# Performance work log

Measured on AMD Instinct MI355X. Metric: run time of the kernel, lower is better.

The kernel has to match this reference:

```python
import jax, jax.numpy as jnp
import numpy as np

N, C, D, H, E, M = 4, 512, 768, 12, 20, 4   # docs, seq, hidden, heads, entities/doc, max mentions
EMB, BLK, L = 768, 64, 97                    # emb_size, block_size, num_labels
P = E * (E - 1)                              # ordered entity pairs per doc
NEG = -1e30


def _forward(seq, attn, mention_start, hts, Wm1, Wm2, bm, Watt, batt, Wpath, bpath,
             Whead, bhead, Wtail, btail, Wbil, bbil):
    def per_doc(seq_i, att_i, pos0, ht):
        pos = pos0 + 1                                            # BERT cls offset
        e_emb = seq_i[pos]                                        # [E,M,D] mention embeddings
        mean_att = att_i.mean(0)                                  # [C,C] head-mean attention
        e_att = jnp.pad(mean_att[pos], ((0, 0), (0, 0), (0, 1)))  # [E,M,C+1] zero pad col
        glob = jax.nn.logsumexp(e_emb, axis=1)                    # [E,D] entity glob emb
        hidx, tidx = ht[:, 0], ht[:, 1]
        hs = e_emb[hidx]; ts = e_emb[tidx]                        # [P,M,D]
        h_att = e_att[hidx]; t_att = e_att[tidx]                  # [P,M,C+1]
        ph = pos[hidx]; pt = pos[tidx]                            # [P,M]
        idx_t = jnp.broadcast_to(pt[:, None, :], (P, M, M))
        idx_h = jnp.broadcast_to(ph[:, None, :], (P, M, M))
        pair_hatt = jnp.take_along_axis(h_att, idx_t, axis=2).mean(1)  # [P,M]
        pair_tatt = jnp.take_along_axis(t_att, idx_h, axis=2).mean(1)
        pair_hatt = pair_hatt / (pair_hatt.sum(1, keepdims=True) + 1e-5)
        pair_tatt = pair_tatt / (pair_tatt.sum(1, keepdims=True) + 1e-5)
        new_hs = jnp.einsum('pm,pmd->pd', pair_tatt, hs)
        new_ts = jnp.einsum('pm,pmd->pd', pair_hatt, ts)
        nh_att = jnp.einsum('pm,pmc->pc', pair_tatt, h_att)
        nt_att = jnp.einsum('pm,pmc->pc', pair_hatt, t_att)
        pa = nh_att * nt_att
        pa = pa / (pa.sum(1, keepdims=True) + 1e-5)
        rs = pa[:, :C] @ seq_i                                    # [P,D] local context
        # RelEdgeLayer over fully-connected entity graph (eval-mode dropout = identity)
        A = glob @ Wm1; B = glob @ Wm2
        edge = jax.nn.relu(A[:, None, :] + B[None, :, :] + bm)    # [E,E,D] edge features
        # path attention: query = cat(hs,ts), targets = cat(e[h,v],e[v,t],e[t,v],e[v,h])
        q = jnp.concatenate([new_hs, new_ts], -1)                 # [P,2D]
        qW = q @ Watt                                             # [P,4D] bilinear half
        q1, q2, q3, q4 = jnp.split(qW, 4, axis=-1)
        E1 = edge[hidx]                                           # edge[h,v]  [P,E,D]
        E2 = jnp.swapaxes(edge[:, tidx], 0, 1)                    # edge[v,t]
        E3 = edge[tidx]                                           # edge[t,v]
        E4 = jnp.swapaxes(edge[:, hidx], 0, 1)                    # edge[v,h]
        score = (jnp.einsum('pd,pvd->pv', q1, E1) + jnp.einsum('pd,pvd->pv', q2, E2)
                 + jnp.einsum('pd,pvd->pv', q3, E3) + jnp.einsum('pd,pvd->pv', q4, E4) + batt)
        v_ids = jnp.arange(E)
        mask = (v_ids[None, :] == hidx[:, None]) | (v_ids[None, :] == tidx[:, None])
        aw = jax.nn.softmax(jnp.where(mask, NEG, score), axis=-1)  # [P,E]
        path = jnp.concatenate([jnp.einsum('pv,pvd->pd', aw, Ek) for Ek in (E1, E2, E3, E4)], -1)
        return new_hs, new_ts, rs, path

    nh, nt, rs, path = jax.vmap(per_doc)(seq, attn, mention_start, hts)
    nh = nh.reshape(-1, D); nt = nt.reshape(-1, D)
    rs = rs.reshape(-1, D); path = path.reshape(-1, 4 * D)
    path = jax.nn.relu(path @ Wpath + bpath)
    hs = jax.nn.relu(jnp.concatenate([nh, rs, path], -1) @ Whead + bhead)
    ts = jax.nn.relu(jnp.concatenate([nt, rs, path], -1) @ Wtail + btail)
    b1 = hs.reshape(-1, EMB // BLK, BLK)
    b2 = ts.reshape(-1, EMB // BLK, BLK)
    bl = (b1[:, :, :, None] * b2[:, :, None, :]).reshape(-1, EMB * BLK)
    return bl @ Wbil + bbil                                       # [N*P, L] logits


def setup_inputs() -> dict:
    key = jax.random.key(0)
    ks = jax.random.split(key, 16)
    s = 0.02
    pairs = np.array([(i, j) for i in range(E) for j in range(E) if i != j], dtype=np.int32)
    return {
        'sequence_output': jax.random.normal(ks[0], (N, C, D), jnp.float32),
        'attention': jax.random.uniform(ks[1], (N, H, C, C), jnp.float32),
        'mention_start': jax.random.randint(ks[2], (N, E, M), 0, C - 2),
        'hts': jnp.broadcast_to(jnp.asarray(pairs), (N, P, 2)),
        'Wm1': jax.random.normal(ks[3], (D, D)) * s,
        'Wm2': jax.random.normal(ks[4], (D, D)) * s,
        'bm': jnp.zeros((D,), jnp.float32),
        'Watt': jax.random.normal(ks[5], (2 * D, 4 * D)) * s,
        'batt': jnp.zeros((), jnp.float32),
        'Wpath': jax.random.normal(ks[6], (4 * D, D)) * s,
        'bpath': jnp.zeros((D,), jnp.float32),
        'Whead': jax.random.normal(ks[7], (3 * D, EMB)) * s,
        'bhead': jnp.zeros((EMB,), jnp.float32),
        'Wtail': jax.random.normal(ks[8], (3 * D, EMB)) * s,
        'btail': jnp.zeros((EMB,), jnp.float32),
        'Wbil': jax.random.normal(ks[9], (EMB * BLK, L)) * s,
        'bbil': jnp.zeros((L,), jnp.float32),
    }


def reference(sequence_output, attention, mention_start, hts, Wm1, Wm2, bm, Watt, batt,
              Wpath, bpath, Whead, bhead, Wtail, btail, Wbil, bbil):
    return _forward(sequence_output, attention, mention_start, hts, Wm1, Wm2, bm, Watt,
                    batt, Wpath, bpath, Whead, bhead, Wtail, btail, Wbil, bbil)
```

## Files before the change

### kernel.cpp

```cpp
#include <hip/hip_runtime.h>
#include <hip/hip_bf16.h>

#define NDOC 4
#define CL   512
#define DD   768
#define HH   12
#define EE   20
#define MM   4
#define PP   380
#define NPAIR 1520
#define LOUT 97
#define KP   40
#define KP2  72

typedef unsigned short u16;
typedef short bf16x8 __attribute__((ext_vector_type(8)));
typedef u16   u16x8  __attribute__((ext_vector_type(8)));
typedef u16   u16x4  __attribute__((ext_vector_type(4)));
typedef float f32x4  __attribute__((ext_vector_type(4)));

#define Z8 (u16x8){0,0,0,0,0,0,0,0}

__device__ __forceinline__ u16 f2bf(float x){
    union { float f; unsigned u; } v; v.f = x;
    return (u16)((v.u + 0x7fffu + ((v.u >> 16) & 1u)) >> 16);
}
__device__ __forceinline__ float bf2f(u16 h){
    union { unsigned u; float f; } v; v.u = ((unsigned)h) << 16;
    return v.f;
}
__device__ __forceinline__ void splitf(float x, u16 &h, u16 &l){
    h = f2bf(x);
    l = f2bf(x - bf2f(h));
}

__global__ __launch_bounds__(256) void k_wsplit(const float* __restrict__ W,
                                                u16* __restrict__ WH, u16* __restrict__ WL,
                                                int K, int N, long long srcStride,
                                                long long dstStride)
{
    __shared__ u16 tH[64][66], tL[64][66];
    const float* Wp = W + (size_t)blockIdx.z*srcStride;
    u16* WHp = WH + (size_t)blockIdx.z*dstStride;
    u16* WLp = WL + (size_t)blockIdx.z*dstStride;
    int n0 = blockIdx.x*64, k0 = blockIdx.y*64;
    int t = threadIdx.x;
    int kr = t>>4, c4 = (t&15)*4;
    bool vec4 = ((N & 3) == 0);
    #pragma unroll
    for (int rr=0; rr<4; ++rr) {
        int k = k0 + kr + rr*16;
        float arr[4];
        if (vec4 && n0 + c4 + 3 < N) {
            float4 v = *(const float4*)(Wp + (size_t)k*N + n0 + c4);
            arr[0]=v.x; arr[1]=v.y; arr[2]=v.z; arr[3]=v.w;
        } else {
            #pragma unroll
            for (int i=0;i<4;++i){ int n=n0+c4+i; arr[i] = (n<N)? Wp[(size_t)k*N+n] : 0.f; }
        }
        #pragma unroll
        for (int i=0;i<4;++i){
            u16 hh,ll; splitf(arr[i],hh,ll);
            tH[c4+i][kr+rr*16] = hh;
            tL[c4+i][kr+rr*16] = ll;
        }
    }
    __syncthreads();
    int nr = t>>4, kc = (t&15)*4;
    #pragma unroll
    for (int rr=0; rr<4; ++rr) {
        int nl = nr + rr*16;
        u16x4 vh, vl;
        #pragma unroll
        for (int i=0;i<4;++i){ vh[i]=tH[nl][kc+i]; vl[i]=tL[nl][kc+i]; }
        size_t o = (size_t)(n0+nl)*K + k0 + kc;
        *(u16x4*)(WHp + o) = vh;
        *(u16x4*)(WLp + o) = vl;
    }
}

__global__ __launch_bounds__(256) void k_prep(const float* __restrict__ att,
                                              const float* __restrict__ seq,
                                              const int* __restrict__ ms,
                                              float* __restrict__ eatt,
                                              float* __restrict__ glob)
{
    int b = blockIdx.x;
    if (b < NDOC*EE*MM) {
        int row = b;
        int i = row / (EE*MM);
        int pos = ms[row] + 1;
        const float* base = att + ((size_t)i*HH)*CL*CL + (size_t)pos*CL;
        for (int c = threadIdx.x; c < CL; c += 256) {
            float s = 0.f;
            #pragma unroll
            for (int h = 0; h < HH; ++h) s += base[(size_t)h*CL*CL + c];
            eatt[(size_t)row*CL + c] = s * (1.0f/HH);
        }
    } else {
        int ie = b - NDOC*EE*MM;
        int i = ie / EE;
        const int* mp = ms + ie*MM;
        const float* sb = seq + (size_t)i*CL*DD;
        const float* r0 = sb + (size_t)(mp[0]+1)*DD;
        const float* r1 = sb + (size_t)(mp[1]+1)*DD;
        const float* r2 = sb + (size_t)(mp[2]+1)*DD;
        const float* r3 = sb + (size_t)(mp[3]+1)*DD;
        for (int d = threadIdx.x; d < DD; d += 256) {
            float a=r0[d], bb=r1[d], c=r2[d], e=r3[d];
            float mx = fmaxf(fmaxf(a,bb), fmaxf(c,e));
            float s = expf(a-mx)+expf(bb-mx)+expf(c-mx)+expf(e-mx);
            glob[(size_t)ie*DD + d] = mx + logf(s);
        }
    }
}

__global__ __launch_bounds__(256) void k_pairvec(const float* __restrict__ seq,
                                                 const float* __restrict__ eatt,
                                                 const int* __restrict__ ms,
                                                 const int* __restrict__ hts,
                                                 u16* __restrict__ nhH, u16* __restrict__ nhL,
                                                 u16* __restrict__ ntH, u16* __restrict__ ntL,
                                                 u16* __restrict__ paH, u16* __restrict__ paL)
{
    int g = blockIdx.x;
    int i = g / PP;
    int h = hts[2*g], t = hts[2*g+1];
    const float* eh = eatt + (size_t)(i*EE+h)*MM*CL;
    const float* et = eatt + (size_t)(i*EE+t)*MM*CL;
    int ph[MM], pt[MM];
    #pragma unroll
    for (int m=0;m<MM;++m){ ph[m]=ms[(i*EE+h)*MM+m]+1; pt[m]=ms[(i*EE+t)*MM+m]+1; }
    float pH[MM], pT[MM]; float sh=0.f, st=0.f;
    #pragma unroll
    for (int m2=0; m2<MM; ++m2) {
        float s = 0.f, s2 = 0.f;
        #pragma unroll
        for (int m=0;m<MM;++m) { s += eh[m*CL + pt[m2]]; s2 += et[m*CL + ph[m2]]; }
        pH[m2] = s*0.25f;  sh += pH[m2];
        pT[m2] = s2*0.25f; st += pT[m2];
    }
    float rh = 1.f/(sh+1e-5f), rt = 1.f/(st+1e-5f);
    #pragma unroll
    for (int m=0;m<MM;++m){ pH[m]*=rh; pT[m]*=rt; }

    const float* sb = seq + (size_t)i*CL*DD;
    for (int d = threadIdx.x; d < DD; d += 256) {
        float nh = pT[0]*sb[(size_t)ph[0]*DD+d] + pT[1]*sb[(size_t)ph[1]*DD+d]
                 + pT[2]*sb[(size_t)ph[2]*DD+d] + pT[3]*sb[(size_t)ph[3]*DD+d];
        float nt = pH[0]*sb[(size_t)pt[0]*DD+d] + pH[1]*sb[(size_t)pt[1]*DD+d]
                 + pH[2]*sb[(size_t)pt[2]*DD+d] + pH[3]*sb[(size_t)pt[3]*DD+d];
        u16 hh,ll;
        splitf(nh,hh,ll);
        nhH[(size_t)g*DD + d]=hh; nhL[(size_t)g*DD + d]=ll;
        splitf(nt,hh,ll);
        ntH[(size_t)g*DD + d]=hh; ntL[(size_t)g*DD + d]=ll;
    }
    float vv[2]; float lsum = 0.f;
    #pragma unroll
    for (int it=0; it<2; ++it) {
        int c = threadIdx.x + it*256;
        float na = pT[0]*eh[c] + pT[1]*eh[CL+c] + pT[2]*eh[2*CL+c] + pT[3]*eh[3*CL+c];
        float nb = pH[0]*et[c] + pH[1]*et[CL+c] + pH[2]*et[2*CL+c] + pH[3]*et[3*CL+c];
        vv[it] = na*nb; lsum += vv[it];
    }
    float tot = lsum;
    #pragma unroll
    for (int o=32;o;o>>=1) tot += __shfl_xor(tot, o);
    __shared__ float wsum[4];
    if ((threadIdx.x & 63)==0) wsum[threadIdx.x>>6] = tot;
    __syncthreads();
    float inv = 1.f/(wsum[0]+wsum[1]+wsum[2]+wsum[3] + 1e-5f);
    #pragma unroll
    for (int it=0; it<2; ++it){
        int c = threadIdx.x + it*256;
        u16 hh,ll; splitf(vv[it]*inv,hh,ll);
        paH[(size_t)g*CL + c]=hh; paL[(size_t)g*CL + c]=ll;
    }
}

__global__ __launch_bounds__(256) void k_edge(const float* __restrict__ Ab,
                                              const float* __restrict__ Bb,
                                              const float* __restrict__ bm,
                                              float* __restrict__ edge)
{
    int iht = blockIdx.x;
    int i = iht/(EE*EE); int rem = iht%(EE*EE); int h = rem/EE; int tt = rem%EE;
    const float* a = Ab + (size_t)(i*EE+h)*DD;
    const float* b = Bb + (size_t)(i*EE+tt)*DD;
    float* e = edge + (size_t)iht*DD;
    for (int d=threadIdx.x; d<DD; d+=256)
        e[d] = fmaxf(a[d]+b[d]+bm[d], 0.f);
}

__global__ __launch_bounds__(256) void k_scorepath(const float* __restrict__ qW,
                                                   const float* __restrict__ edge,
                                                   const int* __restrict__ hts,
                                                   const float* __restrict__ battp,
                                                   u16* __restrict__ pathcH,
                                                   u16* __restrict__ pathcL)
{
    int g = blockIdx.x;
    int i = g / PP;
    int h = hts[2*g], t = hts[2*g+1];
    __shared__ float qs[4*DD];
    __shared__ float sc[EE];
    __shared__ float aw[EE];
    for (int d4 = threadIdx.x; d4 < DD; d4 += 256)
        *(float4*)&qs[d4*4] = *(const float4*)(qW + (size_t)g*3072 + d4*4);
    __syncthreads();
    const float* eb = edge + (size_t)i*EE*EE*DD;
    int lane = threadIdx.x & 63, wid = threadIdx.x >> 6;
    for (int v = wid; v < EE; v += 4) {
        const float* e1 = eb + (size_t)(h*EE+v)*DD;
        const float* e2 = eb + (size_t)(v*EE+t)*DD;
        const float* e3 = eb + (size_t)(t*EE+v)*DD;
        const float* e4 = eb + (size_t)(v*EE+h)*DD;
        float s = 0.f;
        for (int d = lane; d < DD; d += 64)
            s += qs[d]*e1[d] + qs[DD+d]*e2[d] + qs[2*DD+d]*e3[d] + qs[3*DD+d]*e4[d];
        #pragma unroll
        for (int o=32;o;o>>=1) s += __shfl_xor(s, o);
        if (lane==0) sc[v] = s + battp[0];
    }
    __syncthreads();
    if (threadIdx.x == 0) {
        float mx = -3.0e38f;
        for (int v=0;v<EE;++v){ float x = (v==h||v==t)? -1e30f : sc[v]; sc[v]=x; mx = fmaxf(mx,x); }
        float su=0.f;
        for (int v=0;v<EE;++v){ float e = expf(sc[v]-mx); aw[v]=e; su+=e; }
        float inv = 1.f/su;
        for (int v=0;v<EE;++v) aw[v]*=inv;
    }
    __syncthreads();
    for (int idx = threadIdx.x; idx < 4*DD; idx += 256) {
        int k = idx / DD, d = idx % DD;
        const float* e;
        int stride;
        if (k==0)      { e = eb + (size_t)h*EE*DD + d; stride = DD; }
        else if (k==1) { e = eb + (size_t)t*DD + d;     stride = EE*DD; }
        else if (k==2) { e = eb + (size_t)t*EE*DD + d;  stride = DD; }
        else           { e = eb + (size_t)h*DD + d;     stride = EE*DD; }
        float s = 0.f;
        #pragma unroll
        for (int v=0; v<EE; ++v) s += aw[v]*e[(size_t)v*stride];
        u16 hh,ll; splitf(s,hh,ll);
        pathcH[(size_t)g*3072 + idx] = hh;
        pathcL[(size_t)g*3072 + idx] = ll;
    }
}

__global__ __launch_bounds__(256) void gemm_f32s(const float* __restrict__ glob,
                                                 const float* __restrict__ W1,
                                                 const float* __restrict__ W2,
                                                 float* __restrict__ C1,
                                                 float* __restrict__ C2)
{
    int doc = blockIdx.z >> 1, sel = blockIdx.z & 1;
    const float* A = glob + (size_t)doc*EE*DD;
    const float* B = sel ? W2 : W1;
    float* C = (sel ? C2 : C1) + (size_t)doc*EE*DD;
    __shared__ float As[16][68];
    __shared__ float Bs[16][68];
    int n0 = blockIdx.x*64;
    int t = threadIdx.x;
    int tx = t & 15, ty = t >> 4;
    int am = t >> 2, ac = (t & 3) * 4;
    int bk = t >> 4, bn = (t & 15) * 4;
    float acc[4][4] = {};
    for (int k0 = 0; k0 < DD; k0 += 16) {
        float4 av = make_float4(0,0,0,0);
        if (am < EE) av = *reinterpret_cast<const float4*>(A + (size_t)am*DD + k0 + ac);
        As[ac+0][am]=av.x; As[ac+1][am]=av.y; As[ac+2][am]=av.z; As[ac+3][am]=av.w;
        float4 bv = *reinterpret_cast<const float4*>(B + (size_t)(k0+bk)*DD + n0 + bn);
        *reinterpret_cast<float4*>(&Bs[bk][bn]) = bv;
        __syncthreads();
        #pragma unroll
        for (int kk=0; kk<16; ++kk) {
            const float4 a = *reinterpret_cast<const float4*>(&As[kk][ty*4]);
            const float4 b = *reinterpret_cast<const float4*>(&Bs[kk][tx*4]);
            float ar[4] = {a.x,a.y,a.z,a.w};
            float br[4] = {b.x,b.y,b.z,b.w};
            #pragma unroll
            for (int r=0;r<4;++r)
                #pragma unroll
                for (int c2=0;c2<4;++c2) acc[r][c2] = fmaf(ar[r], br[c2], acc[r][c2]);
        }
        __syncthreads();
    }
    #pragma unroll
    for (int r=0;r<4;++r) {
        int gm = ty*4 + r;
        if (gm >= EE) continue;
        #pragma unroll
        for (int c2=0;c2<4;++c2)
            C[(size_t)gm*DD + n0 + tx*4 + c2] = acc[r][c2];
    }
}

enum { MQW=0, MSPLIT=1, MRS=2, MHT=3 };

template<int MODE, int BM, int BN>
__global__ __launch_bounds__(256) void gemm_mfma(
    const u16* __restrict__ aH0, const u16* __restrict__ aL0,
    const u16* __restrict__ aH1, const u16* __restrict__ aL1,
    const u16* __restrict__ aH2, const u16* __restrict__ aL2,
    const u16* __restrict__ a0bH, const u16* __restrict__ a0bL,
    const u16* __restrict__ bH, const u16* __restrict__ bL,
    const u16* __restrict__ bHb, const u16* __restrict__ bLb,
    const float* __restrict__ bias, const float* __restrict__ biasb,
    float* __restrict__ oF,
    u16* __restrict__ oH, u16* __restrict__ oL,
    u16* __restrict__ oHb, u16* __restrict__ oLb,
    int M, int N, int Ktot, int segsz)
{
    constexpr int NWN = BN/64;
    constexpr int NWM = 4/NWN;
    constexpr int WM  = BM/NWM;
    constexpr int MFR = WM/16;
    constexpr int NFR = 4;
    __shared__ u16 AsH[BM*KP], AsL[BM*KP], BsH[BN*KP], BsL[BN*KP];

    const int t = threadIdx.x;
    const int z = blockIdx.z;
    const int m0 = blockIdx.y*BM, n0 = blockIdx.x*BN;
    const int lane = t & 63, wid = t >> 6;
    const int wr = wid / NWN, wc = wid % NWN;
    const int lrow = lane & 15, lg = lane >> 4;

    const u16 *segH0=aH0, *segL0=aL0;
    const u16 *bHp = bH, *bLp = bL;
    const float* bp = bias;
    float* fOut = nullptr;
    u16 *hOut = oH, *lOut = oL;
    int Mloc = M;
    long long outRow0 = 0;
    if constexpr (MODE==MRS) {
        segH0 = aH0 + (size_t)z*PP*CL;  segL0 = aL0 + (size_t)z*PP*CL;
        bHp   = bH  + (size_t)z*DD*CL;  bLp   = bL  + (size_t)z*DD*CL;
        Mloc = PP; outRow0 = (long long)z*PP;
    }
    if constexpr (MODE==MHT) {
        if (z == 0) { fOut = oF; hOut = nullptr; lOut = nullptr; }
        else { segH0 = a0bH; segL0 = a0bL; bHp = bHb; bLp = bLb; bp = biasb;
               hOut = oHb; lOut = oLb; }
    }

    f32x4 acc[MFR][NFR];
    #pragma unroll
    for (int i=0;i<MFR;++i)
        #pragma unroll
        for (int j=0;j<NFR;++j) acc[i][j] = f32x4{0.f,0.f,0.f,0.f};

    const int nkt = Ktot / 32;

    for (int kt = 0; kt < nkt; ++kt) {
        const int k0 = kt*32;
        {
            int seg = (k0 >= 2*segsz) ? 2 : (k0 >= segsz ? 1 : 0);
            int soff = k0 - seg*segsz;
            const u16* pH = (seg==0)?segH0:(seg==1)?aH1:aH2;
            const u16* pL = (seg==0)?segL0:(seg==1)?aL1:aL2;
            if constexpr (BM==128) {
                int row = t>>1, koff = (t&1)*16;
                int gm = m0 + row;
                u16x8 h0=Z8,h1=Z8,l0=Z8,l1=Z8;
                if (gm < Mloc) {
                    const u16* ph = pH + (size_t)gm*segsz + soff + koff;
                    const u16* pl = pL + (size_t)gm*segsz + soff + koff;
                    h0 = *(const u16x8*)ph;  h1 = *(const u16x8*)(ph+8);
                    l0 = *(const u16x8*)pl;  l1 = *(const u16x8*)(pl+8);
                }
                *(u16x8*)&AsH[row*KP + koff]     = h0;
                *(u16x8*)&AsH[row*KP + koff + 8] = h1;
                *(u16x8*)&AsL[row*KP + koff]     = l0;
                *(u16x8*)&AsL[row*KP + koff + 8] = l1;
            } else {
                int row = t>>2, koff = (t&3)*8;
                int gm = m0 + row;
                u16x8 h0=Z8,l0=Z8;
                if (gm < Mloc) {
                    h0 = *(const u16x8*)(pH + (size_t)gm*segsz + soff + koff);
                    l0 = *(const u16x8*)(pL + (size_t)gm*segsz + soff + koff);
                }
                *(u16x8*)&AsH[row*KP + koff] = h0;
                *(u16x8*)&AsL[row*KP + koff] = l0;
            }
        }
        {
            if constexpr (BN==128) {
                int row = t>>1, koff = (t&1)*16;
                const u16* ph = bHp + (size_t)(n0+row)*Ktot + k0 + koff;
                const u16* pl = bLp + (size_t)(n0+row)*Ktot + k0 + koff;
                *(u16x8*)&BsH[row*KP + koff]     = *(const u16x8*)ph;
                *(u16x8*)&BsH[row*KP + koff + 8] = *(const u16x8*)(ph+8);
                *(u16x8*)&BsL[row*KP + koff]     = *(const u16x8*)pl;
                *(u16x8*)&BsL[row*KP + koff + 8] = *(const u16x8*)(pl+8);
            } else {
                int row = t>>2, koff = (t&3)*8;
                *(u16x8*)&BsH[row*KP + koff] = *(const u16x8*)(bHp + (size_t)(n0+row)*Ktot + k0 + koff);
                *(u16x8*)&BsL[row*KP + koff] = *(const u16x8*)(bLp + (size_t)(n0+row)*Ktot + k0 + koff);
            }
        }
        __syncthreads();
        {
            bf16x8 ah[MFR], al[MFR], bh[NFR], bl[NFR];
            #pragma unroll
            for (int mi=0;mi<MFR;++mi){
                int off = (wr*WM + mi*16 + lrow)*KP + lg*8;
                ah[mi] = *(const bf16x8*)&AsH[off];
                al[mi] = *(const bf16x8*)&AsL[off];
            }
            #pragma unroll
            for (int ni=0;ni<NFR;++ni){
                int off = (wc*64 + ni*16 + lrow)*KP + lg*8;
                bh[ni] = *(const bf16x8*)&BsH[off];
                bl[ni] = *(const bf16x8*)&BsL[off];
            }
            #pragma unroll
            for (int mi=0;mi<MFR;++mi)
                #pragma unroll
                for (int ni=0;ni<NFR;++ni){
                    acc[mi][ni] = __builtin_amdgcn_mfma_f32_16x16x32_bf16(ah[mi], bh[ni], acc[mi][ni], 0,0,0);
                    acc[mi][ni] = __builtin_amdgcn_mfma_f32_16x16x32_bf16(al[mi], bh[ni], acc[mi][ni], 0,0,0);
                    acc[mi][ni] = __builtin_amdgcn_mfma_f32_16x16x32_bf16(ah[mi], bl[ni], acc[mi][ni], 0,0,0);
                }
        }
        __syncthreads();
    }
    #pragma unroll
    for (int mi=0;mi<MFR;++mi)
        #pragma unroll
        for (int ni=0;ni<NFR;++ni)
            #pragma unroll
            for (int r=0;r<4;++r){
                int gm = m0 + wr*WM + mi*16 + lg*4 + r;
                int gn = n0 + wc*64 + ni*16 + lrow;
                if (gm >= Mloc) continue;
                float v = acc[mi][ni][r];
                if constexpr (MODE==MQW) {
                    oF[(size_t)gm*N + gn] = v;
                } else if constexpr (MODE==MRS) {
                    u16 hh,ll; splitf(v,hh,ll);
                    oH[(size_t)(outRow0+gm)*DD + gn] = hh;
                    oL[(size_t)(outRow0+gm)*DD + gn] = ll;
                } else {
                    v = fmaxf(v + bp[gn], 0.f);
                    if (fOut) fOut[(size_t)gm*DD + gn] = v;
                    if (hOut) {
                        u16 hh,ll; splitf(v,hh,ll);
                        hOut[(size_t)gm*DD + gn] = hh;
                        lOut[(size_t)gm*DD + gn] = ll;
                    }
                }
            }
}

__global__ __launch_bounds__(256) void k_bil2(const u16* __restrict__ tsH,
                                              const u16* __restrict__ tsL,
                                              const float* __restrict__ hsF,
                                              const u16* __restrict__ WH,
                                              const u16* __restrict__ WL,
                                              float* __restrict__ out)
{
    __shared__ u16 TsH[128*KP2], TsL[128*KP2];
    __shared__ u16 BbH[128*KP], BbL[128*KP];
    const int t = threadIdx.x;
    const int m0 = blockIdx.y*128;
    const int z = blockIdx.z;
    const int j = z>>2, a0 = (z&3)*16;
    const int lane = t & 63, wid = t >> 6;
    const int wr = wid >> 1, wc = wid & 1;
    const int lrow = lane & 15, lg = lane >> 4;

    {
        int row = t>>1, half = t&1;
        int gm = m0 + row;
        int col = j*64 + half*32;
        u16x8 h0=Z8,h1=Z8,h2=Z8,h3=Z8,l0=Z8,l1=Z8,l2=Z8,l3=Z8;
        if (gm < NPAIR) {
            const u16* ph = tsH + (size_t)gm*DD + col;
            const u16* pl = tsL + (size_t)gm*DD + col;
            h0=*(const u16x8*)ph;      h1=*(const u16x8*)(ph+8);
            h2=*(const u16x8*)(ph+16); h3=*(const u16x8*)(ph+24);
            l0=*(const u16x8*)pl;      l1=*(const u16x8*)(pl+8);
            l2=*(const u16x8*)(pl+16); l3=*(const u16x8*)(pl+24);
        }
        int o = row*KP2 + half*32;
        *(u16x8*)&TsH[o]=h0;    *(u16x8*)&TsH[o+8]=h1;
        *(u16x8*)&TsH[o+16]=h2; *(u16x8*)&TsH[o+24]=h3;
        *(u16x8*)&TsL[o]=l0;    *(u16x8*)&TsL[o+8]=l1;
        *(u16x8*)&TsL[o+16]=l2; *(u16x8*)&TsL[o+24]=l3;
    }

    f32x4 facc[4][4];
    #pragma unroll
    for (int mi=0;mi<4;++mi)
        #pragma unroll
        for (int ni=0;ni<4;++ni) facc[mi][ni] = f32x4{0.f,0.f,0.f,0.f};

    for (int ai=0; ai<16; ++ai) {
        int a = a0 + ai;
        f32x4 tacc[4][4];
        #pragma unroll
        for (int mi=0;mi<4;++mi)
            #pragma unroll
            for (int ni=0;ni<4;++ni) tacc[mi][ni] = f32x4{0.f,0.f,0.f,0.f};
        #pragma unroll
        for (int half=0; half<2; ++half) {
            __syncthreads();
            {
                int row = t>>1, h2 = t&1;
                size_t src = (size_t)row*49152 + (size_t)j*4096 + (size_t)a*64 + half*32 + h2*16;
                *(u16x8*)&BbH[row*KP + h2*16]     = *(const u16x8*)(WH + src);
                *(u16x8*)&BbH[row*KP + h2*16 + 8] = *(const u16x8*)(WH + src + 8);
                *(u16x8*)&BbL[row*KP + h2*16]     = *(const u16x8*)(WL + src);
                *(u16x8*)&BbL[row*KP + h2*16 + 8] = *(const u16x8*)(WL + src + 8);
            }
            __syncthreads();
            bf16x8 ah[4], al[4], bh[4], bl[4];
            #pragma unroll
            for (int mi=0;mi<4;++mi){
                int off = (wr*64 + mi*16 + lrow)*KP2 + half*32 + lg*8;
                ah[mi] = *(const bf16x8*)&TsH[off];
                al[mi] = *(const bf16x8*)&TsL[off];
            }
            #pragma unroll
            for (int ni=0;ni<4;++ni){
                int off = (wc*64 + ni*16 + lrow)*KP + lg*8;
                bh[ni] = *(const bf16x8*)&BbH[off];
                bl[ni] = *(const bf16x8*)&BbL[off];
            }
            #pragma unroll
            for (int mi=0;mi<4;++mi)
                #pragma unroll
                for (int ni=0;ni<4;++ni){
                    tacc[mi][ni] = __builtin_amdgcn_mfma_f32_16x16x32_bf16(ah[mi], bh[ni], tacc[mi][ni], 0,0,0);
                    tacc[mi][ni] = __builtin_amdgcn_mfma_f32_16x16x32_bf16(al[mi], bh[ni], tacc[mi][ni], 0,0,0);
                    tacc[mi][ni] = __builtin_amdgcn_mfma_f32_16x16x32_bf16(ah[mi], bl[ni], tacc[mi][ni], 0,0,0);
                }
        }
        float hv[4][4];
        #pragma unroll
        for (int mi=0;mi<4;++mi)
            #pragma unroll
            for (int r=0;r<4;++r){
                int gm = m0 + wr*64 + mi*16 + lg*4 + r;
                hv[mi][r] = (gm < NPAIR) ? hsF[(size_t)gm*DD + j*64 + a] : 0.f;
            }
        #pragma unroll
        for (int mi=0;mi<4;++mi)
            #pragma unroll
            for (int ni=0;ni<4;++ni)
                #pragma unroll
                for (int r=0;r<4;++r)
                    facc[mi][ni][r] = fmaf(hv[mi][r], tacc[mi][ni][r], facc[mi][ni][r]);
    }
    #pragma unroll
    for (int mi=0;mi<4;++mi)
        #pragma unroll
        for (int ni=0;ni<4;++ni)
            #pragma unroll
            for (int r=0;r<4;++r){
                int gm = m0 + wr*64 + mi*16 + lg*4 + r;
                int gn = wc*64 + ni*16 + lrow;
                if (gm < NPAIR && gn < LOUT)
                    atomicAdd(&out[(size_t)gm*LOUT + gn], facc[mi][ni][r]);
            }
}

__global__ __launch_bounds__(256) void k_outinit(const float* __restrict__ bbil,
                                                 float* __restrict__ out)
{
    int idx = blockIdx.x*blockDim.x + threadIdx.x;
    if (idx >= NPAIR*LOUT) return;
    out[idx] = bbil[idx % LOUT];
}

extern "C" void kernel_launch(void* const* d_in, const int* in_sizes, int n_in,
                              void* d_out, int out_size, void* d_ws, size_t ws_size,
                              hipStream_t stream)
{
    (void)in_sizes; (void)n_in; (void)out_size;
    const float* seq   = (const float*)d_in[0];
    const float* att   = (const float*)d_in[1];
    const int*   ms    = (const int*)d_in[2];
    const int*   hts   = (const int*)d_in[3];
    const float* Wm1   = (const float*)d_in[4];
    const float* Wm2   = (const float*)d_in[5];
    const float* bm    = (const float*)d_in[6];
    const float* Watt  = (const float*)d_in[7];
    const float* batt  = (const float*)d_in[8];
    const float* Wpath = (const float*)d_in[9];
    const float* bpath = (const float*)d_in[10];
    const float* Whead = (const float*)d_in[11];
    const float* bhead = (const float*)d_in[12];
    const float* Wtail = (const float*)d_in[13];
    const float* btail = (const float*)d_in[14];
    const float* Wbil  = (const float*)d_in[15];
    const float* bbil  = (const float*)d_in[16];
    float* out = (float*)d_out;

    char* base = (char*)d_ws;
    size_t off = 0;
    auto take = [&](size_t bytes)->char* { char* r = base+off; off += bytes; return r; };
    char*  R0      = base;
    float* edge    = (float*)take(4915200);
    float* qWb     = (float*)take(18677760);
    u16*   pathcH  = (u16*)  take(9338880);
    u16*   pathcL  = (u16*)  take(9338880);
    u16* nhH = (u16*)take(2334720);  u16* nhL = (u16*)take(2334720);
    u16* ntH = (u16*)take(2334720);  u16* ntL = (u16*)take(2334720);
    u16* rsH = (u16*)take(2334720);  u16* rsL = (u16*)take(2334720);
    u16* pthH= (u16*)take(2334720);  u16* pthL= (u16*)take(2334720);
    u16* tsH = (u16*)take(2334720);  u16* tsL = (u16*)take(2334720);
    float* hsF = (float*)take(4669440);
    float* glob = (float*)take(245760);
    float* Abuf = (float*)take(245760);
    float* Bbuf = (float*)take(245760);
    char*  R1     = base+off;
    float* eatt   = (float*)take(655360);
    u16*   paH    = (u16*)  take(1556480);
    u16*   paL    = (u16*)  take(1556480);
    u16*   seqTH  = (u16*)  take(3145728);
    u16*   seqTL  = (u16*)  take(3145728);
    char*  R2     = base+off;
    u16*   WattTH = (u16*)  take(9437184);
    u16*   WattTL = (u16*)  take(9437184);
    size_t peak = off;
    if (peak > ws_size) return;

    u16* WpathTH = (u16*)R1;
    u16* WpathTL = (u16*)(R1 + 4718592);
    u16* WheadTH = (u16*)R2;
    u16* WheadTL = (u16*)(R2 + 3538944);
    u16* WtailTH = (u16*)(R2 + 7077888);
    u16* WtailTL = (u16*)(R2 + 10616832);
    u16* WbilTH  = (u16*)R0;
    u16* WbilTL  = (u16*)(R0 + 12582912);

    k_wsplit<<<dim3(3072/64, 1536/64, 1), 256, 0, stream>>>(Watt, WattTH, WattTL, 1536, 3072, 0, 0);
    k_wsplit<<<dim3(768/64, 512/64, NDOC), 256, 0, stream>>>(seq, seqTH, seqTL, 512, 768,
                                                             (long long)CL*DD, (long long)DD*CL);
    k_prep<<<NDOC*EE*MM + NDOC*EE, 256, 0, stream>>>(att, seq, ms, eatt, glob);
    k_pairvec<<<NPAIR, 256, 0, stream>>>(seq, eatt, ms, hts, nhH, nhL, ntH, ntL, paH, paL);

    gemm_f32s<<<dim3(12, 1, 2*NDOC), 256, 0, stream>>>(glob, Wm1, Wm2, Abuf, Bbuf);
    k_edge<<<NDOC*EE*EE, 256, 0, stream>>>(Abuf, Bbuf, bm, edge);
    k_outinit<<<(NPAIR*LOUT+255)/256, 256, 0, stream>>>(bbil, out);

    gemm_mfma<MRS,64,64><<<dim3(12, 6, NDOC), 256, 0, stream>>>(
        paH, paL, nullptr, nullptr, nullptr, nullptr, nullptr, nullptr,
        seqTH, seqTL, nullptr, nullptr, nullptr, nullptr,
        nullptr, rsH, rsL, nullptr, nullptr, PP, DD, CL, CL);

    k_wsplit<<<dim3(768/64, 3072/64, 1), 256, 0, stream>>>(Wpath, WpathTH, WpathTL, 3072, 768, 0, 0);

    gemm_mfma<MQW,128,128><<<dim3(3072/128, 12, 1), 256, 0, stream>>>(
        nhH, nhL, ntH, ntL, nullptr, nullptr, nullptr, nullptr,
        WattTH, WattTL, nullptr, nullptr, nullptr, nullptr,
        qWb, nullptr, nullptr, nullptr, nullptr, NPAIR, 3072, 1536, DD);

    k_wsplit<<<dim3(768/64, 2304/64, 1), 256, 0, stream>>>(Whead, WheadTH, WheadTL, 2304, 768, 0, 0);
    k_wsplit<<<dim3(768/64, 2304/64, 1), 256, 0, stream>>>(Wtail, WtailTH, WtailTL, 2304, 768, 0, 0);

    k_scorepath<<<NPAIR, 256, 0, stream>>>(qWb, edge, hts, batt, pathcH, pathcL);

    gemm_mfma<MSPLIT,64,64><<<dim3(12, 24, 1), 256, 0, stream>>>(
        pathcH, pathcL, nullptr, nullptr, nullptr, nullptr, nullptr, nullptr,
        WpathTH, WpathTL, nullptr, nullptr, bpath, nullptr,
        nullptr, pthH, pthL, nullptr, nullptr, NPAIR, DD, 3072, 3072);

    k_wsplit<<<dim3(128/64, 49152/64, 1), 256, 0, stream>>>(Wbil, WbilTH, WbilTL, 49152, LOUT, 0, 0);

    gemm_mfma<MHT,64,64><<<dim3(12, 24, 2), 256, 0, stream>>>(
        nhH, nhL, rsH, rsL, pthH, pthL, ntH, ntL,
        WheadTH, WheadTL, WtailTH, WtailTL, bhead, btail,
        hsF, nullptr, nullptr, tsH, tsL, NPAIR, DD, 2304, DD);

    k_bil2<<<dim3(1, 12, 48), 256, 0, stream>>>(tsH, tsL, hsF, WbilTH, WbilTL, out);
}
```

Before: 726.8 us.

## Double-buffer shared tiles with register prefetch in MFMA GEMMs and bilinear kernel

```diff
diff --git a/kernel.cpp b/kernel.cpp
--- a/kernel.cpp
+++ b/kernel.cpp
@@ -300,7 +300,7 @@
 
 enum { MQW=0, MSPLIT=1, MRS=2, MHT=3 };
 
-template<int MODE, int BM, int BN>
+template<int MODE, int BN>
 __global__ __launch_bounds__(256) void gemm_mfma(
     const u16* __restrict__ aH0, const u16* __restrict__ aL0,
     const u16* __restrict__ aH1, const u16* __restrict__ aL1,
@@ -314,12 +314,14 @@
     u16* __restrict__ oHb, u16* __restrict__ oLb,
     int M, int N, int Ktot, int segsz)
 {
+    constexpr int BM  = 128;
     constexpr int NWN = BN/64;
     constexpr int NWM = 4/NWN;
     constexpr int WM  = BM/NWM;
     constexpr int MFR = WM/16;
     constexpr int NFR = 4;
-    __shared__ u16 AsH[BM*KP], AsL[BM*KP], BsH[BN*KP], BsL[BN*KP];
+    __shared__ u16 AsH[2][BM*KP], AsL[2][BM*KP];
+    __shared__ u16 BsH[2][BN*KP], BsL[2][BN*KP];
 
     const int t = threadIdx.x;
     const int z = blockIdx.z;
@@ -354,79 +356,78 @@
 
     const int nkt = Ktot / 32;
 
+    const int arow = t>>1, akoff = (t&1)*16;
+    const int brow = (BN==128)? (t>>1) : (t>>2);
+    const int bkoff = (BN==128)? (t&1)*16 : (t&3)*8;
+
+    u16x8 rah0, rah1, ral0, ral1;
+    u16x8 rbh0, rbh1, rbl0, rbl1;
+
+    auto loadA = [&](int kt){
+        int k0g = kt*32;
+        int seg = (k0g >= 2*segsz) ? 2 : (k0g >= segsz ? 1 : 0);
+        int soff = k0g - seg*segsz;
+        const u16* pH = (seg==0)?segH0:(seg==1)?aH1:aH2;
+        const u16* pL = (seg==0)?segL0:(seg==1)?aL1:aL2;
+        int gm = m0 + arow;
+        rah0=Z8; rah1=Z8; ral0=Z8; ral1=Z8;
+        if (gm < Mloc) {
+            const u16* ph = pH + (size_t)gm*segsz + soff + akoff;
+            const u16* pl = pL + (size_t)gm*segsz + soff + akoff;
+            rah0 = *(const u16x8*)ph;  rah1 = *(const u16x8*)(ph+8);
+            ral0 = *(const u16x8*)pl;  ral1 = *(const u16x8*)(pl+8);
+        }
+    };
+    auto writeA = [&](int b){
+        *(u16x8*)&AsH[b][arow*KP + akoff]     = rah0;
+        *(u16x8*)&AsH[b][arow*KP + akoff + 8] = rah1;
+        *(u16x8*)&AsL[b][arow*KP + akoff]     = ral0;
+        *(u16x8*)&AsL[b][arow*KP + akoff + 8] = ral1;
+    };
+    auto loadB = [&](int kt){
+        int k0g = kt*32;
+        const u16* ph = bHp + (size_t)(n0+brow)*Ktot + k0g + bkoff;
+        const u16* pl = bLp + (size_t)(n0+brow)*Ktot + k0g + bkoff;
+        rbh0 = *(const u16x8*)ph;
+        rbl0 = *(const u16x8*)pl;
+        if constexpr (BN==128) { rbh1 = *(const u16x8*)(ph+8); rbl1 = *(const u16x8*)(pl+8); }
+    };
+    auto writeB = [&](int b){
+        *(u16x8*)&BsH[b][brow*KP + bkoff] = rbh0;
+        *(u16x8*)&BsL[b][brow*KP + bkoff] = rbl0;
+        if constexpr (BN==128) {
+            *(u16x8*)&BsH[b][brow*KP + bkoff + 8] = rbh1;
+            *(u16x8*)&BsL[b][brow*KP + bkoff + 8] = rbl1;
+        }
+    };
+
+    loadA(0); loadB(0);
     for (int kt = 0; kt < nkt; ++kt) {
-        const int k0 = kt*32;
-        {
-            int seg = (k0 >= 2*segsz) ? 2 : (k0 >= segsz ? 1 : 0);
-            int soff = k0 - seg*segsz;
-            const u16* pH = (seg==0)?segH0:(seg==1)?aH1:aH2;
-            const u16* pL = (seg==0)?segL0:(seg==1)?aL1:aL2;
-            if constexpr (BM==128) {
-                int row = t>>1, koff = (t&1)*16;
-                int gm = m0 + row;
-                u16x8 h0=Z8,h1=Z8,l0=Z8,l1=Z8;
-                if (gm < Mloc) {
-                    const u16* ph = pH + (size_t)gm*segsz + soff + koff;
-                    const u16* pl = pL + (size_t)gm*segsz + soff + koff;
-                    h0 = *(const u16x8*)ph;  h1 = *(const u16x8*)(ph+8);
-                    l0 = *(const u16x8*)pl;  l1 = *(const u16x8*)(pl+8);
-                }
-                *(u16x8*)&AsH[row*KP + koff]     = h0;
-                *(u16x8*)&AsH[row*KP + koff + 8] = h1;
-                *(u16x8*)&AsL[row*KP + koff]     = l0;
-                *(u16x8*)&AsL[row*KP + koff + 8] = l1;
-            } else {
-                int row = t>>2, koff = (t&3)*8;
-                int gm = m0 + row;
-                u16x8 h0=Z8,l0=Z8;
-                if (gm < Mloc) {
-                    h0 = *(const u16x8*)(pH + (size_t)gm*segsz + soff + koff);
-                    l0 = *(const u16x8*)(pL + (size_t)gm*segsz + soff + koff);
-                }
-                *(u16x8*)&AsH[row*KP + koff] = h0;
-                *(u16x8*)&AsL[row*KP + koff] = l0;
+        const int cb = kt & 1;
+        writeA(cb); writeB(cb);
+        if (kt+1 < nkt) { loadA(kt+1); loadB(kt+1); }
+        __syncthreads();
+        bf16x8 ah[MFR], al[MFR], bh[NFR], bl[NFR];
+        #pragma unroll
+        for (int mi=0;mi<MFR;++mi){
+            int off = (wr*WM + mi*16 + lrow)*KP + lg*8;
+            ah[mi] = *(const bf16x8*)&AsH[cb][off];
+            al[mi] = *(const bf16x8*)&AsL[cb][off];
+        }
+        #pragma unroll
+        for (int ni=0;ni<NFR;++ni){
+            int off = (wc*64 + ni*16 + lrow)*KP + lg*8;
+            bh[ni] = *(const bf16x8*)&BsH[cb][off];
+            bl[ni] = *(const bf16x8*)&BsL[cb][off];
+        }
+        #pragma unroll
+        for (int mi=0;mi<MFR;++mi)
+            #pragma unroll
+            for (int ni=0;ni<NFR;++ni){
+                acc[mi][ni] = __builtin_amdgcn_mfma_f32_16x16x32_bf16(ah[mi], bh[ni], acc[mi][ni], 0,0,0);
+                acc[mi][ni] = __builtin_amdgcn_mfma_f32_16x16x32_bf16(al[mi], bh[ni], acc[mi][ni], 0,0,0);
+                acc[mi][ni] = __builtin_amdgcn_mfma_f32_16x16x32_bf16(ah[mi], bl[ni], acc[mi][ni], 0,0,0);
             }
-        }
-        {
-            if constexpr (BN==128) {
-                int row = t>>1, koff = (t&1)*16;
-                const u16* ph = bHp + (size_t)(n0+row)*Ktot + k0 + koff;
-                const u16* pl = bLp + (size_t)(n0+row)*Ktot + k0 + koff;
-                *(u16x8*)&BsH[row*KP + koff]     = *(const u16x8*)ph;
-                *(u16x8*)&BsH[row*KP + koff + 8] = *(const u16x8*)(ph+8);
-                *(u16x8*)&BsL[row*KP + koff]     = *(const u16x8*)pl;
-                *(u16x8*)&BsL[row*KP + koff + 8] = *(const u16x8*)(pl+8);
-            } else {
-                int row = t>>2, koff = (t&3)*8;
-                *(u16x8*)&BsH[row*KP + koff] = *(const u16x8*)(bHp + (size_t)(n0+row)*Ktot + k0 + koff);
-                *(u16x8*)&BsL[row*KP + koff] = *(const u16x8*)(bLp + (size_t)(n0+row)*Ktot + k0 + koff);
-            }
-        }
-        __syncthreads();
-        {
-            bf16x8 ah[MFR], al[MFR], bh[NFR], bl[NFR];
-            #pragma unroll
-            for (int mi=0;mi<MFR;++mi){
-                int off = (wr*WM + mi*16 + lrow)*KP + lg*8;
-                ah[mi] = *(const bf16x8*)&AsH[off];
-                al[mi] = *(const bf16x8*)&AsL[off];
-            }
-            #pragma unroll
-            for (int ni=0;ni<NFR;++ni){
-                int off = (wc*64 + ni*16 + lrow)*KP + lg*8;
-                bh[ni] = *(const bf16x8*)&BsH[off];
-                bl[ni] = *(const bf16x8*)&BsL[off];
-            }
-            #pragma unroll
-            for (int mi=0;mi<MFR;++mi)
-                #pragma unroll
-                for (int ni=0;ni<NFR;++ni){
-                    acc[mi][ni] = __builtin_amdgcn_mfma_f32_16x16x32_bf16(ah[mi], bh[ni], acc[mi][ni], 0,0,0);
-                    acc[mi][ni] = __builtin_amdgcn_mfma_f32_16x16x32_bf16(al[mi], bh[ni], acc[mi][ni], 0,0,0);
-                    acc[mi][ni] = __builtin_amdgcn_mfma_f32_16x16x32_bf16(ah[mi], bl[ni], acc[mi][ni], 0,0,0);
-                }
-        }
-        __syncthreads();
     }
     #pragma unroll
     for (int mi=0;mi<MFR;++mi)
@@ -464,7 +465,7 @@
                                               float* __restrict__ out)
 {
     __shared__ u16 TsH[128*KP2], TsL[128*KP2];
-    __shared__ u16 BbH[128*KP], BbL[128*KP];
+    __shared__ u16 BbH[2][128*KP], BbL[2][128*KP];
     const int t = threadIdx.x;
     const int m0 = blockIdx.y*128;
     const int z = blockIdx.z;
@@ -493,68 +494,82 @@
         *(u16x8*)&TsL[o+16]=l2; *(u16x8*)&TsL[o+24]=l3;
     }
 
+    const int brow = t>>1, bsub = t&1;
+    u16x8 rbh0, rbh1, rbl0, rbl1;
+    auto loadB = [&](int it){
+        int a = a0 + (it>>1), half = it&1;
+        size_t src = (size_t)brow*49152 + (size_t)j*4096 + (size_t)a*64 + half*32 + bsub*16;
+        rbh0 = *(const u16x8*)(WH + src);
+        rbh1 = *(const u16x8*)(WH + src + 8);
+        rbl0 = *(const u16x8*)(WL + src);
+        rbl1 = *(const u16x8*)(WL + src + 8);
+    };
+    auto writeB = [&](int b){
+        *(u16x8*)&BbH[b][brow*KP + bsub*16]     = rbh0;
+        *(u16x8*)&BbH[b][brow*KP + bsub*16 + 8] = rbh1;
+        *(u16x8*)&BbL[b][brow*KP + bsub*16]     = rbl0;
+        *(u16x8*)&BbL[b][brow*KP + bsub*16 + 8] = rbl1;
+    };
+
     f32x4 facc[4][4];
     #pragma unroll
     for (int mi=0;mi<4;++mi)
         #pragma unroll
         for (int ni=0;ni<4;++ni) facc[mi][ni] = f32x4{0.f,0.f,0.f,0.f};
 
-    for (int ai=0; ai<16; ++ai) {
-        int a = a0 + ai;
-        f32x4 tacc[4][4];
-        #pragma unroll
-        for (int mi=0;mi<4;++mi)
-            #pragma unroll
-            for (int ni=0;ni<4;++ni) tacc[mi][ni] = f32x4{0.f,0.f,0.f,0.f};
-        #pragma unroll
-        for (int half=0; half<2; ++half) {
-            __syncthreads();
-            {
-                int row = t>>1, h2 = t&1;
-                size_t src = (size_t)row*49152 + (size_t)j*4096 + (size_t)a*64 + half*32 + h2*16;
-                *(u16x8*)&BbH[row*KP + h2*16]     = *(const u16x8*)(WH + src);
-                *(u16x8*)&BbH[row*KP + h2*16 + 8] = *(const u16x8*)(WH + src + 8);
-                *(u16x8*)&BbL[row*KP + h2*16]     = *(const u16x8*)(WL + src);
-                *(u16x8*)&BbL[row*KP + h2*16 + 8] = *(const u16x8*)(WL + src + 8);
-            }
-            __syncthreads();
-            bf16x8 ah[4], al[4], bh[4], bl[4];
-            #pragma unroll
-            for (int mi=0;mi<4;++mi){
-                int off = (wr*64 + mi*16 + lrow)*KP2 + half*32 + lg*8;
-                ah[mi] = *(const bf16x8*)&TsH[off];
-                al[mi] = *(const bf16x8*)&TsL[off];
-            }
-            #pragma unroll
-            for (int ni=0;ni<4;++ni){
-                int off = (wc*64 + ni*16 + lrow)*KP + lg*8;
-                bh[ni] = *(const bf16x8*)&BbH[off];
-                bl[ni] = *(const bf16x8*)&BbL[off];
-            }
+    f32x4 tacc[4][4];
+    loadB(0);
+    for (int it = 0; it < 32; ++it) {
+        const int cb = it & 1;
+        writeB(cb);
+        if (it+1 < 32) loadB(it+1);
+        __syncthreads();
+        if ((it&1)==0) {
             #pragma unroll
             for (int mi=0;mi<4;++mi)
                 #pragma unroll
-                for (int ni=0;ni<4;++ni){
-                    tacc[mi][ni] = __builtin_amdgcn_mfma_f32_16x16x32_bf16(ah[mi], bh[ni], tacc[mi][ni], 0,0,0);
-                    tacc[mi][ni] = __builtin_amdgcn_mfma_f32_16x16x32_bf16(al[mi], bh[ni], tacc[mi][ni], 0,0,0);
-                    tacc[mi][ni] = __builtin_amdgcn_mfma_f32_16x16x32_bf16(ah[mi], bl[ni], tacc[mi][ni], 0,0,0);
+                for (int ni=0;ni<4;++ni) tacc[mi][ni] = f32x4{0.f,0.f,0.f,0.f};
+        }
+        const int half = it&1;
+        bf16x8 ah[4], al[4], bh[4], bl[4];
+        #pragma unroll
+        for (int mi=0;mi<4;++mi){
+            int off = (wr*64 + mi*16 + lrow)*KP2 + half*32 + lg*8;
+            ah[mi] = *(const bf16x8*)&TsH[off];
+            al[mi] = *(const bf16x8*)&TsL[off];
+        }
+        #pragma unroll
+        for (int ni=0;ni<4;++ni){
+            int off = (wc*64 + ni*16 + lrow)*KP + lg*8;
+            bh[ni] = *(const bf16x8*)&BbH[cb][off];
+            bl[ni] = *(const bf16x8*)&BbL[cb][off];
+        }
+        #pragma unroll
+        for (int mi=0;mi<4;++mi)
+            #pragma unroll
+            for (int ni=0;ni<4;++ni){
+                tacc[mi][ni] = __builtin_amdgcn_mfma_f32_16x16x32_bf16(ah[mi], bh[ni], tacc[mi][ni], 0,0,0);
+                tacc[mi][ni] = __builtin_amdgcn_mfma_f32_16x16x32_bf16(al[mi], bh[ni], tacc[mi][ni], 0,0,0);
+                tacc[mi][ni] = __builtin_amdgcn_mfma_f32_16x16x32_bf16(ah[mi], bl[ni], tacc[mi][ni], 0,0,0);
+            }
+        if (it&1) {
+            int a = a0 + (it>>1);
+            float hv[4][4];
+            #pragma unroll
+            for (int mi=0;mi<4;++mi)
+                #pragma unroll
+                for (int r=0;r<4;++r){
+                    int gm = m0 + wr*64 + mi*16 + lg*4 + r;
+                    hv[mi][r] = (gm < NPAIR) ? hsF[(size_t)gm*DD + j*64 + a] : 0.f;
                 }
-        }
-        float hv[4][4];
-        #pragma unroll
-        for (int mi=0;mi<4;++mi)
-            #pragma unroll
-            for (int r=0;r<4;++r){
-                int gm = m0 + wr*64 + mi*16 + lg*4 + r;
-                hv[mi][r] = (gm < NPAIR) ? hsF[(size_t)gm*DD + j*64 + a] : 0.f;
-            }
-        #pragma unroll
-        for (int mi=0;mi<4;++mi)
-            #pragma unroll
-            for (int ni=0;ni<4;++ni)
+            #pragma unroll
+            for (int mi=0;mi<4;++mi)
                 #pragma unroll
-                for (int r=0;r<4;++r)
-                    facc[mi][ni][r] = fmaf(hv[mi][r], tacc[mi][ni][r], facc[mi][ni][r]);
+                for (int ni=0;ni<4;++ni)
+                    #pragma unroll
+                    for (int r=0;r<4;++r)
+                        facc[mi][ni][r] = fmaf(hv[mi][r], tacc[mi][ni][r], facc[mi][ni][r]);
+        }
     }
     #pragma unroll
     for (int mi=0;mi<4;++mi)
@@ -649,14 +664,14 @@
     k_edge<<<NDOC*EE*EE, 256, 0, stream>>>(Abuf, Bbuf, bm, edge);
     k_outinit<<<(NPAIR*LOUT+255)/256, 256, 0, stream>>>(bbil, out);
 
-    gemm_mfma<MRS,64,64><<<dim3(12, 6, NDOC), 256, 0, stream>>>(
+    gemm_mfma<MRS,64><<<dim3(12, 3, NDOC), 256, 0, stream>>>(
         paH, paL, nullptr, nullptr, nullptr, nullptr, nullptr, nullptr,
         seqTH, seqTL, nullptr, nullptr, nullptr, nullptr,
         nullptr, rsH, rsL, nullptr, nullptr, PP, DD, CL, CL);
 
     k_wsplit<<<dim3(768/64, 3072/64, 1), 256, 0, stream>>>(Wpath, WpathTH, WpathTL, 3072, 768, 0, 0);
 
-    gemm_mfma<MQW,128,128><<<dim3(3072/128, 12, 1), 256, 0, stream>>>(
+    gemm_mfma<MQW,128><<<dim3(3072/128, 12, 1), 256, 0, stream>>>(
         nhH, nhL, ntH, ntL, nullptr, nullptr, nullptr, nullptr,
         WattTH, WattTL, nullptr, nullptr, nullptr, nullptr,
         qWb, nullptr, nullptr, nullptr, nullptr, NPAIR, 3072, 1536, DD);
@@ -666,14 +681,14 @@
 
     k_scorepath<<<NPAIR, 256, 0, stream>>>(qWb, edge, hts, batt, pathcH, pathcL);
 
-    gemm_mfma<MSPLIT,64,64><<<dim3(12, 24, 1), 256, 0, stream>>>(
+    gemm_mfma<MSPLIT,64><<<dim3(12, 12, 1), 256, 0, stream>>>(
         pathcH, pathcL, nullptr, nullptr, nullptr, nullptr, nullptr, nullptr,
         WpathTH, WpathTL, nullptr, nullptr, bpath, nullptr,
         nullptr, pthH, pthL, nullptr, nullptr, NPAIR, DD, 3072, 3072);
 
     k_wsplit<<<dim3(128/64, 49152/64, 1), 256, 0, stream>>>(Wbil, WbilTH, WbilTL, 49152, LOUT, 0, 0);
 
-    gemm_mfma<MHT,64,64><<<dim3(12, 24, 2), 256, 0, stream>>>(
+    gemm_mfma<MHT,64><<<dim3(12, 12, 2), 256, 0, stream>>>(
         nhH, nhL, rsH, rsL, pthH, pthL, ntH, ntL,
         WheadTH, WheadTL, WtailTH, WtailTL, bhead, btail,
         hsF, nullptr, nullptr, tsH, tsL, NPAIR, DD, 2304, DD);
```

Measured after the change: 1.343 ms. 1.85x slower.
